# Performance work log

Hardware: AMD Instinct MI355X
Metric: run time of the kernel (lower is better)

Reference implementation:

```python
import jax, jax.numpy as jnp
import numpy as np

EMB = 128
N_TEXT = 80000
N_NODES = 100000
E = 800000
N_REL = 500
PRED_IN = 4 * EMB + 2 * 2 + 2 * 2 * (2 + 2)  # 532


def scatter_mean(x, src, dst, num_nodes):
    # PyG MessagePassing(aggr='mean'): mean of x[src] grouped by dst; empty groups -> 0
    sums = jax.ops.segment_sum(x[src], dst, num_segments=num_nodes)
    cnt = jax.ops.segment_sum(jnp.ones((src.shape[0], 1), x.dtype), dst, num_segments=num_nodes)
    return sums / jnp.maximum(cnt, 1.0)


def setup_inputs() -> dict:
    key = jax.random.key(0)
    ks = jax.random.split(key, 12)
    inp = {
        "h_id_tensor": jax.random.randint(ks[0], (E,), 0, N_NODES),
        "r_id_tensor": jax.random.randint(ks[1], (E,), 0, N_REL),
        "t_id_tensor": jax.random.randint(ks[2], (E,), 0, N_NODES),
        "q_emb": jax.random.normal(ks[3], (1, EMB), jnp.float32),
        "entity_embs": jax.random.normal(ks[4], (N_TEXT, EMB), jnp.float32),
        "num_non_text_entities": N_NODES - N_TEXT,
        "relation_embs": jax.random.normal(ks[5], (N_REL, EMB), jnp.float32),
        "topic_entity_one_hot": jax.random.uniform(ks[6], (N_NODES, 2), jnp.float32),
        # learned params
        "non_text_emb": jax.random.normal(ks[7], (1, EMB), jnp.float32) * 0.02,
        "W1": jax.random.normal(ks[8], (EMB, PRED_IN), jnp.float32) / np.sqrt(PRED_IN),
        "b1": jnp.zeros((EMB,), jnp.float32),
        "W2": jax.random.normal(ks[9], (1, EMB), jnp.float32) / np.sqrt(EMB),
        "b2": jnp.zeros((1,), jnp.float32),
    }
    return inp


def reference(h_id_tensor, r_id_tensor, t_id_tensor, q_emb, entity_embs,
              num_non_text_entities, relation_embs, topic_entity_one_hot,
              non_text_emb, W1, b1, W2, b2):
    num_nodes = entity_embs.shape[0] + num_non_text_entities
    # node embeddings: text entities + shared non-text embedding row
    h_e = jnp.concatenate(
        [entity_embs, jnp.broadcast_to(non_text_emb, (num_non_text_entities, EMB))], axis=0)

    # DDE: forward rounds over (h->t), reverse rounds over (t->h); scatter-mean diffusion
    dde_list = []
    h_pe = topic_entity_one_hot
    for _ in range(2):
        h_pe = scatter_mean(h_pe, h_id_tensor, t_id_tensor, num_nodes)
        dde_list.append(h_pe)
    h_pe_rev = topic_entity_one_hot
    for _ in range(2):
        h_pe_rev = scatter_mean(h_pe_rev, t_id_tensor, h_id_tensor, num_nodes)
        dde_list.append(h_pe_rev)

    h_e_full = jnp.concatenate([h_e, topic_entity_one_hot] + dde_list, axis=1)  # [N, EMB+10]

    h_r = relation_embs[r_id_tensor]                       # [E, EMB]
    h_q = jnp.broadcast_to(q_emb, (h_r.shape[0], EMB))     # [E, EMB]
    h_triple = jnp.concatenate(
        [h_q, h_e_full[h_id_tensor], h_r, h_e_full[t_id_tensor]], axis=1)  # [E, PRED_IN]

    hidden = jax.nn.relu(h_triple @ W1.T + b1)             # [E, EMB]
    pred = hidden @ W2.T + b2                              # [E, 1]
    return pred
```

## Files before the change

### kernel.cpp

```cpp
#include <hip/hip_runtime.h>

#define EMB 128
#define W1LD 532
#define KP 160
#define ST 264
#define BSH 9
#define BNODES 512
#define EPB 4096

typedef unsigned long long u64;
typedef unsigned int u32;
typedef unsigned short u16;
typedef __attribute__((ext_vector_type(8))) short short8;
typedef __attribute__((ext_vector_type(4))) float f32x4;
typedef _Float16 h2 __attribute__((ext_vector_type(2)));

__device__ __forceinline__ u16 f2bf(float x) {
    unsigned u = __float_as_uint(x);
    unsigned r = (u + 0x7fffu + ((u >> 16) & 1u)) >> 16;
    return (u16)r;
}
__device__ __forceinline__ u16 f2h(float x) {
    union { _Float16 h; u16 u; } c; c.h = (_Float16)x; return c.u;
}
__device__ __forceinline__ h2 u2h(unsigned u) {
    union { unsigned u; h2 h; } c; c.u = u; return c.h;
}

__device__ __forceinline__ float ep8(const uint4& ua, const uint4& ub,
                                     const uint4& ur, const uint4& uw, float s) {
    const h2 z = {(_Float16)0.0f, (_Float16)0.0f};
#define EP1(c)                                                         \
    {                                                                  \
        h2 x = u2h(ua.c) + u2h(ur.c) + u2h(ub.c);                      \
        x = __builtin_elementwise_max(x, z);                           \
        h2 w = u2h(uw.c);                                              \
        _Pragma("clang diagnostic push")                               \
        s = FDOT2(x, w, s);                                            \
        _Pragma("clang diagnostic pop")                                \
    }
#if __has_builtin(__builtin_amdgcn_fdot2)
#define FDOT2(x, w, s) __builtin_amdgcn_fdot2(x, w, s, false)
#else
#define FDOT2(x, w, s) (s + (float)x[0] * (float)w[0] + (float)x[1] * (float)w[1])
#endif
    EP1(x) EP1(y) EP1(z) EP1(w)
#undef EP1
#undef FDOT2
    return s;
}

__global__ __launch_bounds__(1024) void khist(
    const int* __restrict__ h_id, const int* __restrict__ t_id,
    u32* __restrict__ hist, int E, int NBKT, int NSB)
{
    __shared__ u32 lh[512];
    const int t = threadIdx.x, sb = blockIdx.x;
    const int rows = 2 * NBKT;
    if (t < rows) lh[t] = 0;
    __syncthreads();
    const int base = sb * EPB;
#pragma unroll
    for (int c = 0; c < EPB / 1024; c++) {
        int e = base + c * 1024 + t;
        if (e < E) {
            atomicAdd(&lh[t_id[e] >> BSH], 1u);
            atomicAdd(&lh[NBKT + (h_id[e] >> BSH)], 1u);
        }
    }
    __syncthreads();
    if (t < rows) hist[t * NSB + sb] = lh[t];
}

__global__ __launch_bounds__(256) void kscanA(
    u32* __restrict__ hist, u32* __restrict__ tot, int NSB)
{
    __shared__ u32 s[256];
    const int t = threadIdx.x, row = blockIdx.x;
    u32 v = (t < NSB) ? hist[row * NSB + t] : 0;
    s[t] = v;
    __syncthreads();
    for (int o = 1; o < 256; o <<= 1) {
        u32 x = (t >= o) ? s[t - o] : 0;
        __syncthreads();
        s[t] += x;
        __syncthreads();
    }
    if (t < NSB) hist[row * NSB + t] = s[t] - v;
    if (t == 255) tot[row] = s[255];
}

__global__ __launch_bounds__(1024) void kplace(
    const int* __restrict__ h_id, const int* __restrict__ r_id,
    const int* __restrict__ t_id,
    const u32* __restrict__ hist, const u32* __restrict__ tot,
    u32* __restrict__ bstart,
    u32* __restrict__ perm_t, u64* __restrict__ perm_e,
    int E, int NBKT, int NSB)
{
    __shared__ u32 cur[512];
    const int t = threadIdx.x, sb = blockIdx.x;
    const int rows = 2 * NBKT;
    if (t < rows) {
        const int b0 = (t < NBKT) ? 0 : NBKT;
        u32 base = 0;
        for (int b = b0; b < t; b++) base += tot[b];
        cur[t] = base + hist[t * NSB + sb];
        if (sb == 0) {
            const int seg = (t < NBKT) ? 0 : (NBKT + 1);
            bstart[seg + (t - b0)] = base;
            if (t == b0) bstart[seg + NBKT] = (u32)E;
        }
    }
    __syncthreads();
    const int ebase = sb * EPB;
#pragma unroll
    for (int c = 0; c < EPB / 1024; c++) {
        int e = ebase + c * 1024 + t;
        if (e < E) {
            int tt = t_id[e], h = h_id[e], r = r_id[e];
            u32 pt = atomicAdd(&cur[tt >> BSH], 1u);
            perm_t[pt] = (u32)h | ((u32)(tt & (BNODES - 1)) << 17);
            u32 ph = atomicAdd(&cur[NBKT + (h >> BSH)], 1u);
            perm_e[ph] = (u64)h | ((u64)tt << 17) | ((u64)r << 34)
                       | ((u64)e << 43);
        }
    }
}

template<int ROUND>
__global__ __launch_bounds__(256) void kscat(
    const u32* __restrict__ perm_t, const u64* __restrict__ perm_e,
    const u32* __restrict__ bstart,
    const float* __restrict__ topic,
    const float* __restrict__ src_t, const float* __restrict__ src_h,
    float* __restrict__ out_t, float* __restrict__ out_h,
    const float* __restrict__ W1, const float* __restrict__ q,
    const float* __restrict__ rel, const float* __restrict__ b1,
    const float* __restrict__ W2,
    u16* __restrict__ WBF, float* __restrict__ qWb,
    u16* __restrict__ W2h, u16* __restrict__ Rbf,
    int N, int NBKT, int NREL)
{
    const int bid = blockIdx.x, t = threadIdx.x;
    if (bid < 2 * NBKT) {
        __shared__ u64 acc[BNODES];
        const int d = (bid < NBKT) ? 0 : 1;
        const int b = bid - d * NBKT;
        const float* srcv = (ROUND == 1) ? topic : (d ? src_h : src_t);
        float* out = d ? out_h : out_t;

        for (int i = t; i < BNODES; i += 256) acc[i] = 0;
        __syncthreads();
        const u32 s0 = bstart[d * (NBKT + 1) + b];
        const u32 s1 = bstart[d * (NBKT + 1) + b + 1];
        if (d == 0) {
            for (u32 i = s0 + t; i < s1; i += 256) {
                u32 rec  = perm_t[i];
                u32 src  = rec & 0x1FFFFu;
                u32 slot = rec >> 17;
                float2 v = *(const float2*)(srcv + 2 * src);
                u64 p = (u64)__float2uint_rn(v.x * 1048576.0f)
                      | ((u64)__float2uint_rn(v.y * 1048576.0f) << 26)
                      | (1ull << 52);
                atomicAdd(&acc[slot], p);
            }
        } else {
            for (u32 i = s0 + t; i < s1; i += 256) {
                u64 rec  = perm_e[i];
                u32 src  = (u32)(rec >> 17) & 0x1FFFFu;
                u32 slot = (u32)rec & (BNODES - 1);
                float2 v = *(const float2*)(srcv + 2 * src);
                u64 p = (u64)__float2uint_rn(v.x * 1048576.0f)
                      | ((u64)__float2uint_rn(v.y * 1048576.0f) << 26)
                      | (1ull << 52);
                atomicAdd(&acc[slot], p);
            }
        }
        __syncthreads();
        for (int i = t; i < BNODES; i += 256) {
            int node = b * BNODES + i;
            if (node < N) {
                u64 a = acc[i];
                float cnt = (float)(u32)(a >> 52);
                float inv = (1.0f / 1048576.0f) / fmaxf(cnt, 1.0f);
                float2 m;
                m.x = (float)(u32)(a & 0x3FFFFFFu) * inv;
                m.y = (float)(u32)((a >> 26) & 0x3FFFFFFu) * inv;
                *(float2*)(out + 2 * node) = m;
            }
        }
        return;
    }
    if (ROUND != 1) return;
    const int pb = bid - 2 * NBKT;
    if (pb < KP) {
        int k = pb, n = t;
        float v = 0.0f;
        if (k < 138) {
            v = (n < 128) ? W1[(size_t)n * W1LD + 128 + k]
                          : W1[(size_t)(n - 128) * W1LD + 394 + k];
        }
        int kstep = k >> 5, quad = (k >> 3) & 3, j = k & 7;
        WBF[(((size_t)(kstep * 4 + quad) * 256 + n) << 3) + j] = f2bf(v);
        return;
    }
    int b = pb - KP;
    __shared__ float v[EMB];
    if (t < EMB) v[t] = (b == 0) ? q[t] : rel[(size_t)(b - 1) * EMB + t];
    __syncthreads();
    if (t < EMB) {
        const float* w = W1 + (size_t)t * W1LD + (b == 0 ? 0 : 266);
        float s = 0.0f;
#pragma unroll
        for (int k = 0; k < EMB; k += 4) {
            float4 wv = *(const float4*)(w + k);
            s += wv.x * v[k] + wv.y * v[k + 1] + wv.z * v[k + 2] + wv.w * v[k + 3];
        }
        if (b == 0) { qWb[t] = s + b1[t]; W2h[t] = f2h(W2[t]); }
        else        Rbf[(size_t)(b - 1) * EMB + t] = f2h(s);
    }
}

__global__ __launch_bounds__(256) void k2b_node(
    const float* __restrict__ ent, const float* __restrict__ nte,
    const float* __restrict__ topic,
    const float* __restrict__ dde1f, const float* __restrict__ dde2f,
    const float* __restrict__ dde3f, const float* __restrict__ dde4f,
    const u16* __restrict__ WBF, const float* __restrict__ qWb,
    u16* __restrict__ A, u16* __restrict__ B,
    int NT, int N)
{
    __shared__ __align__(16) u16 lds[32 * ST];
    const int t = threadIdx.x;
    const int lane = t & 63;
    const int w    = t >> 6;
    const int ln15 = lane & 15;
    const int quad = lane >> 4;
    const int m0   = (w & 1) * 16;
    const int n0   = (w >> 1) * 128;
    const int nblk = blockIdx.x * 32;

    {
        int m  = t >> 3;
        int kq = (t & 7) << 4;
        int gn = nblk + m;
        const float* src = (gn < N) ? ((gn < NT) ? ent + (size_t)gn * EMB + kq
                                                 : nte + kq)
                                    : nte;
        u16 pk[16];
#pragma unroll
        for (int p = 0; p < 4; p++) {
            float4 v = (gn < N) ? *(const float4*)(src + 4 * p)
                                : make_float4(0.f, 0.f, 0.f, 0.f);
            pk[4 * p + 0] = f2bf(v.x); pk[4 * p + 1] = f2bf(v.y);
            pk[4 * p + 2] = f2bf(v.z); pk[4 * p + 3] = f2bf(v.w);
        }
        *(uint4*)&lds[m * ST + kq]     = *(uint4*)&pk[0];
        *(uint4*)&lds[m * ST + kq + 8] = *(uint4*)&pk[8];
    }
    if (t < 32) {
        int gn = nblk + t;
        if (gn < N) {
            float2 tp = *(const float2*)(topic + 2 * gn);
            float2 d1 = *(const float2*)(dde1f + 2 * gn);
            float2 d2 = *(const float2*)(dde2f + 2 * gn);
            float2 d3 = *(const float2*)(dde3f + 2 * gn);
            float2 d4 = *(const float2*)(dde4f + 2 * gn);
            lds[t * ST + 128] = f2bf(tp.x); lds[t * ST + 129] = f2bf(tp.y);
            lds[t * ST + 130] = f2bf(d1.x); lds[t * ST + 131] = f2bf(d1.y);
            lds[t * ST + 132] = f2bf(d2.x); lds[t * ST + 133] = f2bf(d2.y);
            lds[t * ST + 134] = f2bf(d3.x); lds[t * ST + 135] = f2bf(d3.y);
            lds[t * ST + 136] = f2bf(d4.x); lds[t * ST + 137] = f2bf(d4.y);
        } else {
#pragma unroll
            for (int z = 128; z < 138; z++) lds[t * ST + z] = 0;
        }
#pragma unroll
        for (int z = 138; z < KP; z++) lds[t * ST + z] = 0;
    }
    __syncthreads();

    f32x4 acc[8];
#pragma unroll
    for (int i = 0; i < 8; i++) acc[i] = (f32x4){0.f, 0.f, 0.f, 0.f};

    const u16* wbbase = WBF + (((size_t)quad * 256 + n0 + ln15) << 3);
#pragma unroll
    for (int ks = 0; ks < 5; ks++) {
        short8 a = *(const short8*)&lds[(m0 + ln15) * ST + ks * 32 + quad * 8];
        const u16* wb = wbbase + ((size_t)ks * 4 * 256 * 8);
#pragma unroll
        for (int nt = 0; nt < 8; nt++) {
            short8 b = *(const short8*)(wb + (nt << 7));
            acc[nt] = __builtin_amdgcn_mfma_f32_16x16x32_bf16(a, b, acc[nt], 0, 0, 0);
        }
    }

    __syncthreads();
#pragma unroll
    for (int nt = 0; nt < 8; nt++) {
        int c = n0 + nt * 16 + ln15;
        float qv = (n0 == 0) ? qWb[c] : 0.0f;
#pragma unroll
        for (int r = 0; r < 4; r++) {
            int row = m0 + quad * 4 + r;
            lds[row * ST + c] = f2h(acc[nt][r] + qv);
        }
    }
    __syncthreads();
    {
        int m  = t >> 3;
        int c0 = (t & 7) * 32;
        int gn = nblk + m;
        if (gn < N) {
            uint4 v0 = *(uint4*)&lds[m * ST + c0];
            uint4 v1 = *(uint4*)&lds[m * ST + c0 + 8];
            uint4 v2 = *(uint4*)&lds[m * ST + c0 + 16];
            uint4 v3 = *(uint4*)&lds[m * ST + c0 + 24];
            u16* dst = (c0 < 128) ? (A + (size_t)gn * EMB + c0)
                                  : (B + (size_t)gn * EMB + (c0 - 128));
            ((uint4*)dst)[0] = v0;
            ((uint4*)dst)[1] = v1;
            ((uint4*)dst)[2] = v2;
            ((uint4*)dst)[3] = v3;
        }
    }
}

__global__ __launch_bounds__(256) void edge_pred_srt(
    const u64* __restrict__ perm_e,
    const u16* __restrict__ A, const u16* __restrict__ B,
    const u16* __restrict__ Rbf, const u16* __restrict__ W2h,
    const float* __restrict__ b2, float* __restrict__ out, int E)
{
    const int t    = threadIdx.x;
    const int lane = t & 63;
    const int g    = lane >> 4;
    const int k    = lane & 15;
    const int wv   = t >> 6;
    const int i    = blockIdx.x * 16 + wv * 4 + g;
    const bool valid = i < E;

    const uint4 uw = *(const uint4*)(W2h + k * 8);
    float s = 0.0f;
    u32 e = 0;
    if (valid) {
        u64 rec = perm_e[i];
        u32 h  = (u32)rec & 0x1FFFFu;
        u32 tt = (u32)(rec >> 17) & 0x1FFFFu;
        u32 r  = (u32)(rec >> 34) & 0x1FFu;
        e = (u32)(rec >> 43);
        const uint4 ua = *(const uint4*)(A + (size_t)h * EMB + k * 8);
        const uint4 ub = *(const uint4*)(B + (size_t)tt * EMB + k * 8);
        const uint4 ur = *(const uint4*)(Rbf + (size_t)r * EMB + k * 8);
        s = ep8(ua, ub, ur, uw, 0.0f);
    }
    s += __shfl_xor(s, 1, 64);
    s += __shfl_xor(s, 2, 64);
    s += __shfl_xor(s, 4, 64);
    s += __shfl_xor(s, 8, 64);
    if (k == 0 && valid) out[e] = s + b2[0];
}

__global__ __launch_bounds__(256) void edge_pred_f16(
    const int* __restrict__ h_id, const int* __restrict__ r_id,
    const int* __restrict__ t_id,
    const u16* __restrict__ A, const u16* __restrict__ B,
    const u16* __restrict__ Rbf, const u16* __restrict__ W2h,
    const float* __restrict__ b2, float* __restrict__ out, int E)
{
    const int t    = threadIdx.x;
    const int lane = t & 63;
    const int g    = lane >> 4;
    const int k    = lane & 15;
    const int wv   = t >> 6;
    const int e    = blockIdx.x * 16 + wv * 4 + g;

    const uint4 uw = *(const uint4*)(W2h + k * 8);
    float s = 0.0f;
    if (e < E) {
        const int h = h_id[e], r = r_id[e], tt = t_id[e];
        const uint4 ua = *(const uint4*)(A + (size_t)h * EMB + k * 8);
        const uint4 ub = *(const uint4*)(B + (size_t)tt * EMB + k * 8);
        const uint4 ur = *(const uint4*)(Rbf + (size_t)r * EMB + k * 8);
        s = ep8(ua, ub, ur, uw, 0.0f);
    }
    s += __shfl_xor(s, 1, 64);
    s += __shfl_xor(s, 2, 64);
    s += __shfl_xor(s, 4, 64);
    s += __shfl_xor(s, 8, 64);
    if (k == 0 && e < E) out[e] = s + b2[0];
}


extern "C" void kernel_launch(void* const* d_in, const int* in_sizes, int n_in,
                              void* d_out, int out_size, void* d_ws, size_t ws_size,
                              hipStream_t stream)
{
    const int*   h_id  = (const int*)d_in[0];
    const int*   r_id  = (const int*)d_in[1];
    const int*   t_id  = (const int*)d_in[2];
    const float* q_emb = (const float*)d_in[3];
    const float* ent   = (const float*)d_in[4];
    const float* rel   = (const float*)d_in[6];
    const float* topic = (const float*)d_in[7];
    const float* nte   = (const float*)d_in[8];
    const float* W1    = (const float*)d_in[9];
    const float* b1    = (const float*)d_in[10];
    const float* W2    = (const float*)d_in[11];
    const float* b2    = (const float*)d_in[12];

    const int E    = in_sizes[0];
    const int NT   = in_sizes[4] / EMB;
    const int N    = in_sizes[7] / 2;
    const int NREL = in_sizes[6] / EMB;

    const int NBKT = (N + BNODES - 1) >> BSH;
    const int NSB  = (E + EPB - 1) / EPB;

    float* qWb  = (float*)d_ws;
    u16* W2h    = (u16*)(qWb + EMB);
    u16* Rbf    = W2h + EMB;
    u16* WBF    = Rbf + (size_t)NREL * EMB;
    float* dde1f = (float*)(WBF + (size_t)KP * 256);
    float* dde2f = dde1f + 2 * (size_t)N;
    float* dde3f = dde2f + 2 * (size_t)N;
    float* dde4f = dde3f + 2 * (size_t)N;
    u16* Aw = (u16*)(dde4f + 2 * (size_t)N);
    u16* Bw = Aw + (size_t)N * EMB;
    u64* perm_ded = (u64*)(Bw + (size_t)N * EMB);

    u32* hist   = (u32*)Aw;
    u32* tot    = hist + (size_t)2 * NBKT * NSB;
    u32* bstart = tot + 2 * NBKT;
    u32* perm_t = bstart + 2 * (NBKT + 1);
    u64* perm_alias = (u64*)(((size_t)(perm_t + E) + 7) & ~(size_t)7);

    size_t need_srt = (size_t)((char*)(perm_ded + E) - (char*)d_ws);
    const bool srt = (ws_size >= need_srt) && (E < (1 << 20)) &&
                     (N <= (1 << 17)) && (NREL <= (1 << 9)) && (NSB <= 256);
    u64* perm_e = srt ? perm_ded : perm_alias;

    const int nn = (N + 31) / 32;

    khist<<<NSB, 1024, 0, stream>>>(h_id, t_id, hist, E, NBKT, NSB);
    kscanA<<<2 * NBKT, 256, 0, stream>>>(hist, tot, NSB);
    kplace<<<NSB, 1024, 0, stream>>>(h_id, r_id, t_id, hist, tot, bstart,
                                     perm_t, perm_e, E, NBKT, NSB);

    kscat<1><<<2 * NBKT + KP + 1 + NREL, 256, 0, stream>>>(
        perm_t, perm_e, bstart, topic, nullptr, nullptr, dde1f, dde3f,
        W1, q_emb, rel, b1, W2, WBF, qWb, W2h, Rbf, N, NBKT, NREL);

    kscat<2><<<2 * NBKT, 256, 0, stream>>>(
        perm_t, perm_e, bstart, topic, dde1f, dde3f, dde2f, dde4f,
        W1, q_emb, rel, b1, W2, WBF, qWb, W2h, Rbf, N, NBKT, NREL);

    k2b_node<<<nn, 256, 0, stream>>>(
        ent, nte, topic, dde1f, dde2f, dde3f, dde4f,
        WBF, qWb, Aw, Bw, NT, N);

    if (srt) {
        edge_pred_srt<<<(E + 15) / 16, 256, 0, stream>>>(
            perm_e, Aw, Bw, Rbf, W2h, b2, (float*)d_out, E);
    } else {
        edge_pred_f16<<<(E + 15) / 16, 256, 0, stream>>>(
            h_id, r_id, t_id, Aw, Bw, Rbf, W2h, b2, (float*)d_out, E);
    }
}
```

Measured before the change: 249.0 us.

## Halve bucket size, fold scan into placement, batch four edges per edge-pred group

Bucket size drops from 512 to 256 nodes, which doubles the number of scatter blocks. The separate scan kernel is removed, and each placement block now recomputes the per-bucket totals and prefix sums itself. The edge-prediction kernel processes four sorted edges per 16-lane group so more gathers are in flight per lane. The fused scan trades one launch for redundant per-block work over all histogram rows (each of NSB blocks reads the full histogram), and smaller buckets add histogram rows.

```diff
diff --git a/kernel.cpp b/kernel.cpp
--- a/kernel.cpp
+++ b/kernel.cpp
@@ -4,8 +4,8 @@
 #define W1LD 532
 #define KP 160
 #define ST 264
-#define BSH 9
-#define BNODES 512
+#define BSH 8
+#define BNODES 256
 #define EPB 4096
 
 typedef unsigned long long u64;
@@ -30,20 +30,18 @@
 __device__ __forceinline__ float ep8(const uint4& ua, const uint4& ub,
                                      const uint4& ur, const uint4& uw, float s) {
     const h2 z = {(_Float16)0.0f, (_Float16)0.0f};
+#if __has_builtin(__builtin_amdgcn_fdot2)
+#define FDOT2(x, w, s) __builtin_amdgcn_fdot2(x, w, s, false)
+#else
+#define FDOT2(x, w, s) (s + (float)x[0] * (float)w[0] + (float)x[1] * (float)w[1])
+#endif
 #define EP1(c)                                                         \
     {                                                                  \
         h2 x = u2h(ua.c) + u2h(ur.c) + u2h(ub.c);                      \
         x = __builtin_elementwise_max(x, z);                           \
         h2 w = u2h(uw.c);                                              \
-        _Pragma("clang diagnostic push")                               \
         s = FDOT2(x, w, s);                                            \
-        _Pragma("clang diagnostic pop")                                \
-    }
-#if __has_builtin(__builtin_amdgcn_fdot2)
-#define FDOT2(x, w, s) __builtin_amdgcn_fdot2(x, w, s, false)
-#else
-#define FDOT2(x, w, s) (s + (float)x[0] * (float)w[0] + (float)x[1] * (float)w[1])
-#endif
+    }
     EP1(x) EP1(y) EP1(z) EP1(w)
 #undef EP1
 #undef FDOT2
@@ -54,10 +52,10 @@
     const int* __restrict__ h_id, const int* __restrict__ t_id,
     u32* __restrict__ hist, int E, int NBKT, int NSB)
 {
-    __shared__ u32 lh[512];
+    __shared__ u32 lh[1024];
     const int t = threadIdx.x, sb = blockIdx.x;
     const int rows = 2 * NBKT;
-    if (t < rows) lh[t] = 0;
+    for (int i = t; i < rows; i += 1024) lh[i] = 0;
     __syncthreads();
     const int base = sb * EPB;
 #pragma unroll
@@ -69,43 +67,45 @@
         }
     }
     __syncthreads();
-    if (t < rows) hist[t * NSB + sb] = lh[t];
-}
-
-__global__ __launch_bounds__(256) void kscanA(
-    u32* __restrict__ hist, u32* __restrict__ tot, int NSB)
-{
-    __shared__ u32 s[256];
-    const int t = threadIdx.x, row = blockIdx.x;
-    u32 v = (t < NSB) ? hist[row * NSB + t] : 0;
-    s[t] = v;
-    __syncthreads();
-    for (int o = 1; o < 256; o <<= 1) {
-        u32 x = (t >= o) ? s[t - o] : 0;
-        __syncthreads();
-        s[t] += x;
-        __syncthreads();
-    }
-    if (t < NSB) hist[row * NSB + t] = s[t] - v;
-    if (t == 255) tot[row] = s[255];
-}
-
-__global__ __launch_bounds__(1024) void kplace(
+    for (int i = t; i < rows; i += 1024) hist[(size_t)i * NSB + sb] = lh[i];
+}
+
+__global__ __launch_bounds__(1024) void kplace2(
     const int* __restrict__ h_id, const int* __restrict__ r_id,
     const int* __restrict__ t_id,
-    const u32* __restrict__ hist, const u32* __restrict__ tot,
-    u32* __restrict__ bstart,
+    const u32* __restrict__ hist, u32* __restrict__ bstart,
     u32* __restrict__ perm_t, u64* __restrict__ perm_e,
     int E, int NBKT, int NSB)
 {
-    __shared__ u32 cur[512];
+    __shared__ u32 sc[1024];
+    __shared__ u32 exl[1024];
+    __shared__ u32 cur[1024];
     const int t = threadIdx.x, sb = blockIdx.x;
     const int rows = 2 * NBKT;
+
+    u32 myTot = 0, myPre = 0;
+    if (t < rows) {
+        const u32* hr = hist + (size_t)t * NSB;
+        for (int s = 0; s < NSB; s++) {
+            u32 v = hr[s];
+            myTot += v;
+            myPre += (s < sb) ? v : 0;
+        }
+    }
+    sc[t] = (t < rows) ? myTot : 0;
+    __syncthreads();
+    for (int o = 1; o < 1024; o <<= 1) {
+        u32 x = (t >= o) ? sc[t - o] : 0;
+        __syncthreads();
+        sc[t] += x;
+        __syncthreads();
+    }
+    exl[t] = sc[t] - ((t < rows) ? myTot : 0);
+    __syncthreads();
     if (t < rows) {
         const int b0 = (t < NBKT) ? 0 : NBKT;
-        u32 base = 0;
-        for (int b = b0; b < t; b++) base += tot[b];
-        cur[t] = base + hist[t * NSB + sb];
+        u32 base = exl[t] - ((t < NBKT) ? 0u : exl[NBKT]);
+        cur[t] = base + myPre;
         if (sb == 0) {
             const int seg = (t < NBKT) ? 0 : (NBKT + 1);
             bstart[seg + (t - b0)] = base;
@@ -125,6 +125,86 @@
             perm_e[ph] = (u64)h | ((u64)tt << 17) | ((u64)r << 34)
                        | ((u64)e << 43);
         }
+    }
+}
+
+__device__ __forceinline__ void scat_bucket(
+    int d, int b, const u32* perm_t, const u64* perm_e, const u32* bstart,
+    const float* srcv, float* out, int N, int NBKT, u64* acc)
+{
+    const int t = threadIdx.x;
+    for (int i = t; i < BNODES; i += 256) acc[i] = 0;
+    __syncthreads();
+    const u32 s0 = bstart[d * (NBKT + 1) + b];
+    const u32 s1 = bstart[d * (NBKT + 1) + b + 1];
+    if (d == 0) {
+        for (u32 i = s0 + t; i < s1; i += 256) {
+            u32 rec  = perm_t[i];
+            u32 src  = rec & 0x1FFFFu;
+            u32 slot = rec >> 17;
+            float2 v = *(const float2*)(srcv + 2 * src);
+            u64 p = (u64)__float2uint_rn(v.x * 1048576.0f)
+                  | ((u64)__float2uint_rn(v.y * 1048576.0f) << 26)
+                  | (1ull << 52);
+            atomicAdd(&acc[slot], p);
+        }
+    } else {
+        for (u32 i = s0 + t; i < s1; i += 256) {
+            u64 rec  = perm_e[i];
+            u32 src  = (u32)(rec >> 17) & 0x1FFFFu;
+            u32 slot = (u32)rec & (BNODES - 1);
+            float2 v = *(const float2*)(srcv + 2 * src);
+            u64 p = (u64)__float2uint_rn(v.x * 1048576.0f)
+                  | ((u64)__float2uint_rn(v.y * 1048576.0f) << 26)
+                  | (1ull << 52);
+            atomicAdd(&acc[slot], p);
+        }
+    }
+    __syncthreads();
+    for (int i = t; i < BNODES; i += 256) {
+        int node = b * BNODES + i;
+        if (node < N) {
+            u64 a = acc[i];
+            float cnt = (float)(u32)(a >> 52);
+            float inv = (1.0f / 1048576.0f) / fmaxf(cnt, 1.0f);
+            float2 m;
+            m.x = (float)(u32)(a & 0x3FFFFFFu) * inv;
+            m.y = (float)(u32)((a >> 26) & 0x3FFFFFFu) * inv;
+            *(float2*)(out + 2 * node) = m;
+        }
+    }
+}
+
+__device__ __forceinline__ void prep_block(
+    int pb, const float* W1, const float* q, const float* rel,
+    const float* b1, const float* W2,
+    u16* WBF, float* qWb, u16* W2h, u16* Rbf, float* v )
+{
+    const int t = threadIdx.x;
+    if (pb < KP) {
+        int k = pb, n = t;
+        float val = 0.0f;
+        if (k < 138) {
+            val = (n < 128) ? W1[(size_t)n * W1LD + 128 + k]
+                            : W1[(size_t)(n - 128) * W1LD + 394 + k];
+        }
+        int kstep = k >> 5, quad = (k >> 3) & 3, j = k & 7;
+        WBF[(((size_t)(kstep * 4 + quad) * 256 + n) << 3) + j] = f2bf(val);
+        return;
+    }
+    int b = pb - KP;
+    if (t < EMB) v[t] = (b == 0) ? q[t] : rel[(size_t)(b - 1) * EMB + t];
+    __syncthreads();
+    if (t < EMB) {
+        const float* w = W1 + (size_t)t * W1LD + (b == 0 ? 0 : 266);
+        float s = 0.0f;
+#pragma unroll
+        for (int k = 0; k < EMB; k += 4) {
+            float4 wv = *(const float4*)(w + k);
+            s += wv.x * v[k] + wv.y * v[k + 1] + wv.z * v[k + 2] + wv.w * v[k + 3];
+        }
+        if (b == 0) { qWb[t] = s + b1[t]; W2h[t] = f2h(W2[t]); }
+        else        Rbf[(size_t)(b - 1) * EMB + t] = f2h(s);
     }
 }
 
@@ -142,84 +222,18 @@
     u16* __restrict__ W2h, u16* __restrict__ Rbf,
     int N, int NBKT, int NREL)
 {
-    const int bid = blockIdx.x, t = threadIdx.x;
+    const int bid = blockIdx.x;
     if (bid < 2 * NBKT) {
         __shared__ u64 acc[BNODES];
         const int d = (bid < NBKT) ? 0 : 1;
-        const int b = bid - d * NBKT;
         const float* srcv = (ROUND == 1) ? topic : (d ? src_h : src_t);
-        float* out = d ? out_h : out_t;
-
-        for (int i = t; i < BNODES; i += 256) acc[i] = 0;
-        __syncthreads();
-        const u32 s0 = bstart[d * (NBKT + 1) + b];
-        const u32 s1 = bstart[d * (NBKT + 1) + b + 1];
-        if (d == 0) {
-            for (u32 i = s0 + t; i < s1; i += 256) {
-                u32 rec  = perm_t[i];
-                u32 src  = rec & 0x1FFFFu;
-                u32 slot = rec >> 17;
-                float2 v = *(const float2*)(srcv + 2 * src);
-                u64 p = (u64)__float2uint_rn(v.x * 1048576.0f)
-                      | ((u64)__float2uint_rn(v.y * 1048576.0f) << 26)
-                      | (1ull << 52);
-                atomicAdd(&acc[slot], p);
-            }
-        } else {
-            for (u32 i = s0 + t; i < s1; i += 256) {
-                u64 rec  = perm_e[i];
-                u32 src  = (u32)(rec >> 17) & 0x1FFFFu;
-                u32 slot = (u32)rec & (BNODES - 1);
-                float2 v = *(const float2*)(srcv + 2 * src);
-                u64 p = (u64)__float2uint_rn(v.x * 1048576.0f)
-                      | ((u64)__float2uint_rn(v.y * 1048576.0f) << 26)
-                      | (1ull << 52);
-                atomicAdd(&acc[slot], p);
-            }
-        }
-        __syncthreads();
-        for (int i = t; i < BNODES; i += 256) {
-            int node = b * BNODES + i;
-            if (node < N) {
-                u64 a = acc[i];
-                float cnt = (float)(u32)(a >> 52);
-                float inv = (1.0f / 1048576.0f) / fmaxf(cnt, 1.0f);
-                float2 m;
-                m.x = (float)(u32)(a & 0x3FFFFFFu) * inv;
-                m.y = (float)(u32)((a >> 26) & 0x3FFFFFFu) * inv;
-                *(float2*)(out + 2 * node) = m;
-            }
-        }
+        scat_bucket(d, bid - d * NBKT, perm_t, perm_e, bstart,
+                    srcv, d ? out_h : out_t, N, NBKT, acc);
         return;
     }
     if (ROUND != 1) return;
-    const int pb = bid - 2 * NBKT;
-    if (pb < KP) {
-        int k = pb, n = t;
-        float v = 0.0f;
-        if (k < 138) {
-            v = (n < 128) ? W1[(size_t)n * W1LD + 128 + k]
-                          : W1[(size_t)(n - 128) * W1LD + 394 + k];
-        }
-        int kstep = k >> 5, quad = (k >> 3) & 3, j = k & 7;
-        WBF[(((size_t)(kstep * 4 + quad) * 256 + n) << 3) + j] = f2bf(v);
-        return;
-    }
-    int b = pb - KP;
     __shared__ float v[EMB];
-    if (t < EMB) v[t] = (b == 0) ? q[t] : rel[(size_t)(b - 1) * EMB + t];
-    __syncthreads();
-    if (t < EMB) {
-        const float* w = W1 + (size_t)t * W1LD + (b == 0 ? 0 : 266);
-        float s = 0.0f;
-#pragma unroll
-        for (int k = 0; k < EMB; k += 4) {
-            float4 wv = *(const float4*)(w + k);
-            s += wv.x * v[k] + wv.y * v[k + 1] + wv.z * v[k + 2] + wv.w * v[k + 3];
-        }
-        if (b == 0) { qWb[t] = s + b1[t]; W2h[t] = f2h(W2[t]); }
-        else        Rbf[(size_t)(b - 1) * EMB + t] = f2h(s);
-    }
+    prep_block(bid - 2 * NBKT, W1, q, rel, b1, W2, WBF, qWb, W2h, Rbf, v);
 }
 
 __global__ __launch_bounds__(256) void k2b_node(
@@ -328,7 +342,7 @@
     }
 }
 
-__global__ __launch_bounds__(256) void edge_pred_srt(
+__global__ __launch_bounds__(256) void edge_pred_srt4(
     const u64* __restrict__ perm_e,
     const u16* __restrict__ A, const u16* __restrict__ B,
     const u16* __restrict__ Rbf, const u16* __restrict__ W2h,
@@ -339,28 +353,40 @@
     const int g    = lane >> 4;
     const int k    = lane & 15;
     const int wv   = t >> 6;
-    const int i    = blockIdx.x * 16 + wv * 4 + g;
-    const bool valid = i < E;
+    const int i0   = (blockIdx.x * 16 + wv * 4 + g) * 4;
 
     const uint4 uw = *(const uint4*)(W2h + k * 8);
-    float s = 0.0f;
-    u32 e = 0;
-    if (valid) {
-        u64 rec = perm_e[i];
-        u32 h  = (u32)rec & 0x1FFFFu;
-        u32 tt = (u32)(rec >> 17) & 0x1FFFFu;
-        u32 r  = (u32)(rec >> 34) & 0x1FFu;
-        e = (u32)(rec >> 43);
-        const uint4 ua = *(const uint4*)(A + (size_t)h * EMB + k * 8);
-        const uint4 ub = *(const uint4*)(B + (size_t)tt * EMB + k * 8);
-        const uint4 ur = *(const uint4*)(Rbf + (size_t)r * EMB + k * 8);
-        s = ep8(ua, ub, ur, uw, 0.0f);
-    }
-    s += __shfl_xor(s, 1, 64);
-    s += __shfl_xor(s, 2, 64);
-    s += __shfl_xor(s, 4, 64);
-    s += __shfl_xor(s, 8, 64);
-    if (k == 0 && valid) out[e] = s + b2[0];
+    const float bb = b2[0];
+
+    u64 rec[4];
+    bool val[4];
+#pragma unroll
+    for (int j = 0; j < 4; j++) {
+        val[j] = (i0 + j) < E;
+        rec[j] = val[j] ? perm_e[i0 + j] : 0;
+    }
+    uint4 ua[4], ub[4], ur[4];
+#pragma unroll
+    for (int j = 0; j < 4; j++) {
+        u32 h  = (u32)rec[j] & 0x1FFFFu;
+        u32 tt = (u32)(rec[j] >> 17) & 0x1FFFFu;
+        u32 r  = (u32)(rec[j] >> 34) & 0x1FFu;
+        ua[j] = *(const uint4*)(A + (size_t)h * EMB + k * 8);
+        ub[j] = *(const uint4*)(B + (size_t)tt * EMB + k * 8);
+        ur[j] = *(const uint4*)(Rbf + (size_t)r * EMB + k * 8);
+    }
+    float s[4];
+#pragma unroll
+    for (int j = 0; j < 4; j++) s[j] = ep8(ua[j], ub[j], ur[j], uw, 0.0f);
+#pragma unroll
+    for (int j = 0; j < 4; j++) {
+        float v = s[j];
+        v += __shfl_xor(v, 1, 64);
+        v += __shfl_xor(v, 2, 64);
+        v += __shfl_xor(v, 4, 64);
+        v += __shfl_xor(v, 8, 64);
+        if (k == 0 && val[j]) out[(u32)(rec[j] >> 43)] = v + bb;
+    }
 }
 
 __global__ __launch_bounds__(256) void edge_pred_f16(
@@ -432,22 +458,21 @@
     u64* perm_ded = (u64*)(Bw + (size_t)N * EMB);
 
     u32* hist   = (u32*)Aw;
-    u32* tot    = hist + (size_t)2 * NBKT * NSB;
-    u32* bstart = tot + 2 * NBKT;
+    u32* bstart = hist + (size_t)2 * NBKT * NSB;
     u32* perm_t = bstart + 2 * (NBKT + 1);
     u64* perm_alias = (u64*)(((size_t)(perm_t + E) + 7) & ~(size_t)7);
 
     size_t need_srt = (size_t)((char*)(perm_ded + E) - (char*)d_ws);
     const bool srt = (ws_size >= need_srt) && (E < (1 << 20)) &&
-                     (N <= (1 << 17)) && (NREL <= (1 << 9)) && (NSB <= 256);
+                     (N <= (1 << 17)) && (NREL <= (1 << 9)) &&
+                     (2 * NBKT <= 1024);
     u64* perm_e = srt ? perm_ded : perm_alias;
 
     const int nn = (N + 31) / 32;
 
     khist<<<NSB, 1024, 0, stream>>>(h_id, t_id, hist, E, NBKT, NSB);
-    kscanA<<<2 * NBKT, 256, 0, stream>>>(hist, tot, NSB);
-    kplace<<<NSB, 1024, 0, stream>>>(h_id, r_id, t_id, hist, tot, bstart,
-                                     perm_t, perm_e, E, NBKT, NSB);
+    kplace2<<<NSB, 1024, 0, stream>>>(h_id, r_id, t_id, hist, bstart,
+                                      perm_t, perm_e, E, NBKT, NSB);
 
     kscat<1><<<2 * NBKT + KP + 1 + NREL, 256, 0, stream>>>(
         perm_t, perm_e, bstart, topic, nullptr, nullptr, dde1f, dde3f,
@@ -462,7 +487,7 @@
         WBF, qWb, Aw, Bw, NT, N);
 
     if (srt) {
-        edge_pred_srt<<<(E + 15) / 16, 256, 0, stream>>>(
+        edge_pred_srt4<<<(E + 63) / 64, 256, 0, stream>>>(
             perm_e, Aw, Bw, Rbf, W2h, b2, (float*)d_out, E);
     } else {
         edge_pred_f16<<<(E + 15) / 16, 256, 0, stream>>>(
```

New measurement: 312.8 us. 1.26x slower.
